# Kernel optimization log

Hardware: AMD Instinct MI355X
Metric: run time of the kernel (lower is better)

## Reference

```python
import jax, jax.numpy as jnp
import numpy as np

N_NODES = 100000
N_EDGES = 1600000
IN_C = 128
HID = 128
OUT_C = 10
NUM_GRAPHS = 512


def _glorot(key, shape):
    lim = float(np.sqrt(6.0 / (shape[0] + shape[1])))
    return jax.random.uniform(key, shape, jnp.float32, -lim, lim)


def setup_inputs() -> dict:
    key = jax.random.key(0)
    ks = jax.random.split(key, 12)
    x = jax.random.normal(ks[0], (N_NODES, IN_C), jnp.float32)
    edge_index = jax.random.randint(ks[1], (2, N_EDGES), 0, N_NODES, jnp.int64)
    batch = jnp.sort(jax.random.randint(ks[2], (N_NODES,), 0, NUM_GRAPHS, jnp.int64))
    return {
        'x': x, 'edge_index': edge_index, 'batch': batch,
        'Wc0': _glorot(ks[3], (IN_C, HID)), 'bc0': jnp.zeros((HID,), jnp.float32),
        'Wc1': _glorot(ks[4], (HID, HID)), 'bc1': jnp.zeros((HID,), jnp.float32),
        'Wc2': _glorot(ks[5], (HID, HID)), 'bc2': jnp.zeros((HID,), jnp.float32),
        'W1': _glorot(ks[6], (HID, HID)), 'b1': jnp.zeros((HID,), jnp.float32),
        'W2': _glorot(ks[7], (HID, OUT_C)), 'b2': jnp.zeros((OUT_C,), jnp.float32),
    }


def _gcn_conv(x, src, dst, W, b, n):
    # PyG GCNConv: add self-loops, symmetric norm D^-1/2 (A+I) D^-1/2, then XW + b.
    # deg includes the self-loop (+1); messages flow src -> dst.
    deg = jax.ops.segment_sum(jnp.ones((src.shape[0],), x.dtype), dst, num_segments=n) + 1.0
    dinv = jax.lax.rsqrt(deg)  # deg >= 1 so no zeros
    h = x @ W  # [N, H]
    coef = dinv[src] * dinv[dst]  # [E]
    agg = jax.ops.segment_sum(h[src] * coef[:, None], dst, num_segments=n)
    agg = agg + h * (dinv * dinv)[:, None]  # self-loop contribution, no edge materialization
    return agg + b


def reference(x, edge_index, batch, Wc0, bc0, Wc1, bc1, Wc2, bc2, W1, b1, W2, b2):
    n = x.shape[0]
    src, dst = edge_index[0], edge_index[1]
    # eval mode: dropout is identity
    h = jax.nn.relu(_gcn_conv(x, src, dst, Wc0, bc0, n))
    h = jax.nn.relu(_gcn_conv(h, src, dst, Wc1, bc1, n))
    h = _gcn_conv(h, src, dst, Wc2, bc2, n)
    # global_mean_pool over graphs
    sums = jax.ops.segment_sum(h, batch, num_segments=NUM_GRAPHS)
    counts = jax.ops.segment_sum(jnp.ones((n,), h.dtype), batch, num_segments=NUM_GRAPHS)
    pooled = sums / jnp.maximum(counts, 1.0)[:, None]  # [G, H]
    out = jax.nn.relu(pooled @ W1 + b1)
    return out @ W2 + b2  # [G, OUT_C]
```

## Files before the change

### kernel.cpp

```cpp
#include <hip/hip_runtime.h>
#include <hip/hip_bf16.h>
#include <stdint.h>

#define HID     128
#define OUTC    10
#define NGRAPH  512
#define NGROUP  64
#define PSIZE   256
#define CAP     160

using bf16x8 = __attribute__((ext_vector_type(8))) short;
using f32x4  = __attribute__((ext_vector_type(4))) float;

__device__ __forceinline__ short f2bf(float f) {
    __hip_bfloat16 h = __float2bfloat16(f);
    return *reinterpret_cast<short*>(&h);
}
__device__ __forceinline__ float bf2f(short s) {
    union { uint32_t u; float f; } x; x.u = ((uint32_t)(uint16_t)s) << 16; return x.f;
}
__device__ __forceinline__ float bflo(uint32_t v) {
    union { uint32_t u; float f; } x; x.u = v << 16; return x.f;
}
__device__ __forceinline__ float bfhi(uint32_t v) {
    union { uint32_t u; float f; } x; x.u = v & 0xffff0000u; return x.f;
}
__device__ __forceinline__ uint32_t pk2(float lo, float hi) {
    return (uint32_t)(uint16_t)f2bf(lo) | ((uint32_t)(uint16_t)f2bf(hi) << 16);
}

__global__ void detect64_kernel(const int* __restrict__ ei, int* __restrict__ flag) {
    int lane = threadIdx.x & 63;
    int v = ei[2 * lane + 1];
    unsigned long long b = __ballot(v == 0);
    if (threadIdx.x == 0) *flag = (b == ~0ULL) ? 1 : 0;
}

__device__ __forceinline__ int fetch_idx(const int* __restrict__ p, long j, int f64) {
    return p[f64 ? (j << 1) : j];
}

__global__ void __launch_bounds__(256) bin_scatter_kernel(
        const int* __restrict__ ei, const int* __restrict__ flag,
        int* __restrict__ cnt, uint32_t* __restrict__ binned,
        long E, int NBIN, int NBINP) {
    const int group = blockIdx.x & (NGROUP - 1);
    const int f = *flag;
    const long stride = (long)gridDim.x * blockDim.x;
    for (long e = (long)blockIdx.x * blockDim.x + threadIdx.x; e < E; e += stride) {
        int s = fetch_idx(ei, e, f);
        int d = fetch_idx(ei, E + e, f);
        int b = d >> 8;
        int pos = atomicAdd(&cnt[group * NBINP + b], 1);
        if (pos < CAP)
            binned[((size_t)group * NBIN + b) * CAP + pos] =
                (uint32_t)s | ((uint32_t)(d & (PSIZE - 1)) << 20);
    }
}

__global__ void bintot_kernel(const int* __restrict__ cnt, int* __restrict__ bin_tot,
                              int NBIN, int NBINP) {
    int b = blockIdx.x * blockDim.x + threadIdx.x;
    if (b < NBIN) {
        int s = 0;
#pragma unroll
        for (int g = 0; g < NGROUP; ++g) s += cnt[g * NBINP + b];
        bin_tot[b] = s;
    }
}

__global__ void __launch_bounds__(1024) scan_kernel(const int* __restrict__ deg,
                                                    int* __restrict__ ofs, int n) {
    __shared__ int wsum[16];
    __shared__ int carry_s;
    __shared__ int chunk_tot;
    const int tid  = threadIdx.x;
    const int lane = tid & 63;
    const int wid  = tid >> 6;
    if (tid == 0) carry_s = 0;
    __syncthreads();
    const int CHUNK = 4096;
    for (int base = 0; base < n; base += CHUNK) {
        int idx = base + tid * 4;
        int v[4];
#pragma unroll
        for (int j = 0; j < 4; ++j) v[j] = (idx + j < n) ? deg[idx + j] : 0;
        int s1 = v[0] + v[1] + v[2] + v[3];
        int inc = s1;
#pragma unroll
        for (int d = 1; d < 64; d <<= 1) {
            int t = __shfl_up(inc, d, 64);
            if (lane >= d) inc += t;
        }
        if (lane == 63) wsum[wid] = inc;
        __syncthreads();
        if (wid == 0) {
            int ws = (lane < 16) ? wsum[lane] : 0;
            int winc = ws;
#pragma unroll
            for (int d = 1; d < 16; d <<= 1) {
                int t = __shfl_up(winc, d, 64);
                if (lane >= d) winc += t;
            }
            if (lane == 15) chunk_tot = winc;
            if (lane < 16) wsum[lane] = winc - ws;
        }
        __syncthreads();
        int excl = carry_s + wsum[wid] + (inc - s1);
        int run = excl;
#pragma unroll
        for (int j = 0; j < 4; ++j) {
            if (idx + j < n) ofs[idx + j] = run;
            run += v[j];
        }
        __syncthreads();
        if (tid == 0) carry_s += chunk_tot;
        __syncthreads();
    }
    if (tid == 0) ofs[n] = carry_s;
}

__global__ void __launch_bounds__(512) bin_build_kernel(
        const uint32_t* __restrict__ binned, const int* __restrict__ cnt,
        const int* __restrict__ bofs, int* __restrict__ ofs,
        float* __restrict__ dinv, int* __restrict__ col,
        int n, int NBIN, int NBINP, long E) {
    __shared__ int lcnt[PSIZE];
    __shared__ int lofs[PSIZE];
    __shared__ int lrank[PSIZE];
    __shared__ int wtot[4];
    const int b    = blockIdx.x;
    const int v0   = b * PSIZE;
    const int nn   = min(PSIZE, n - v0);
    const int tid  = threadIdx.x;
    const int wv   = tid >> 6;
    const int lane = tid & 63;
    if (tid < PSIZE) { lcnt[tid] = 0; lrank[tid] = 0; }
    __syncthreads();
#pragma unroll
    for (int sg = wv; sg < NGROUP; sg += 8) {
        const int c = min(cnt[sg * NBINP + b], CAP);
        const uint32_t* __restrict__ src = binned + ((size_t)sg * NBIN + b) * CAP;
        for (int i = lane; i < c; i += 64)
            atomicAdd(&lcnt[src[i] >> 20], 1);
    }
    __syncthreads();
    if (tid < PSIZE) {
        int v = lcnt[tid];
        int inc = v;
#pragma unroll
        for (int d = 1; d < 64; d <<= 1) {
            int t = __shfl_up(inc, d, 64);
            if (lane >= d) inc += t;
        }
        if (lane == 63) wtot[wv] = inc;
        lofs[tid] = inc - v;
    }
    __syncthreads();
    if (tid < PSIZE) {
        int add = 0;
#pragma unroll
        for (int k = 0; k < 4; ++k) if (k < wv) add += wtot[k];
        lofs[tid] += add;
    }
    __syncthreads();
    const int base = bofs[b];
#pragma unroll
    for (int sg = wv; sg < NGROUP; sg += 8) {
        const int c = min(cnt[sg * NBINP + b], CAP);
        const uint32_t* __restrict__ src = binned + ((size_t)sg * NBIN + b) * CAP;
        for (int i = lane; i < c; i += 64) {
            uint32_t v = src[i];
            int dl = (int)(v >> 20);
            int rk = atomicAdd(&lrank[dl], 1);
            col[base + lofs[dl] + rk] = (int)(v & 0xFFFFFu);
        }
    }
    if (tid < nn) {
        ofs[v0 + tid]  = base + lofs[tid];
        dinv[v0 + tid] = rsqrtf((float)lcnt[tid] + 1.0f);
    }
    if (tid == 0 && v0 + nn == n) ofs[n] = (int)E;
}

__global__ void __launch_bounds__(128) wprep_kernel(
        const float* __restrict__ W0, const float* __restrict__ W1,
        const float* __restrict__ W2, short* __restrict__ Wt) {
    const float* W = (blockIdx.x == 0) ? W0 : (blockIdx.x == 1) ? W1 : W2;
    short* hi = Wt + (size_t)blockIdx.x * 2 * HID * HID;
    short* lo = hi + HID * HID;
    __shared__ float Ws[64][129];
    const int t = threadIdx.x;
    for (int half = 0; half < 2; ++half) {
        const int kbase = half * 64;
#pragma unroll
        for (int it = 0; it < 16; ++it) {
            int idx = (t + it * 128) * 4;
            int k = idx >> 7, c = idx & 127;
            float4 v = *(const float4*)(W + (size_t)(kbase + k) * HID + c);
            Ws[k][c] = v.x; Ws[k][c + 1] = v.y; Ws[k][c + 2] = v.z; Ws[k][c + 3] = v.w;
        }
        __syncthreads();
        for (int it = 0; it < 64; ++it) {
            int k2 = t & 63;
            int c  = (t >> 6) + it * 2;
            float w = Ws[k2][c];
            short h = f2bf(w);
            hi[(size_t)c * HID + kbase + k2] = h;
            lo[(size_t)c * HID + kbase + k2] = f2bf(w - bf2f(h));
        }
        __syncthreads();
    }
}

template<bool AFP32>
__global__ void __launch_bounds__(256) gemm_hs_kernel(
        const void* __restrict__ Ap, const short* __restrict__ Wt,
        const float* __restrict__ dinv, short* __restrict__ hs, int n) {
    const short* __restrict__ Bh = Wt;
    const short* __restrict__ Bl = Wt + HID * HID;
    const int tid = threadIdx.x;
    const int w  = tid >> 6;
    const int l  = tid & 63;
    const int lr = l & 15;
    const int kq = l >> 4;
    const int r0 = blockIdx.x * 128;

    f32x4 acc[8][2] = {};
    const int col0 = w * 32 + lr;
    const int col1 = w * 32 + 16 + lr;

    const float* Af = (const float*)Ap;
    const short* Ab = (const short*)Ap;

#pragma unroll
    for (int ks = 0; ks < 4; ++ks) {
        const int k0 = ks * 32 + kq * 8;
        bf16x8 a[8];
#pragma unroll
        for (int rf = 0; rf < 8; ++rf) {
            int row = r0 + rf * 16 + lr;
            if (row >= n) row = n - 1;
            if (AFP32) {
                const float* ap = Af + (size_t)row * HID + k0;
                float4 f0 = *(const float4*)ap;
                float4 f1 = *(const float4*)(ap + 4);
                bf16x8 tv;
                tv[0] = f2bf(f0.x); tv[1] = f2bf(f0.y); tv[2] = f2bf(f0.z); tv[3] = f2bf(f0.w);
                tv[4] = f2bf(f1.x); tv[5] = f2bf(f1.y); tv[6] = f2bf(f1.z); tv[7] = f2bf(f1.w);
                a[rf] = tv;
            } else {
                a[rf] = *(const bf16x8*)(Ab + (size_t)row * HID + k0);
            }
        }
        bf16x8 bh0 = *(const bf16x8*)(Bh + (size_t)col0 * HID + k0);
        bf16x8 bh1 = *(const bf16x8*)(Bh + (size_t)col1 * HID + k0);
        bf16x8 bl0 = *(const bf16x8*)(Bl + (size_t)col0 * HID + k0);
        bf16x8 bl1 = *(const bf16x8*)(Bl + (size_t)col1 * HID + k0);
#pragma unroll
        for (int rf = 0; rf < 8; ++rf) {
            acc[rf][0] = __builtin_amdgcn_mfma_f32_16x16x32_bf16(a[rf], bh0, acc[rf][0], 0, 0, 0);
            acc[rf][1] = __builtin_amdgcn_mfma_f32_16x16x32_bf16(a[rf], bh1, acc[rf][1], 0, 0, 0);
            acc[rf][0] = __builtin_amdgcn_mfma_f32_16x16x32_bf16(a[rf], bl0, acc[rf][0], 0, 0, 0);
            acc[rf][1] = __builtin_amdgcn_mfma_f32_16x16x32_bf16(a[rf], bl1, acc[rf][1], 0, 0, 0);
        }
    }
#pragma unroll
    for (int rf = 0; rf < 8; ++rf) {
#pragma unroll
        for (int rg = 0; rg < 4; ++rg) {
            int row = r0 + rf * 16 + kq * 4 + rg;
            if (row < n) {
                float dn = dinv[row];
                hs[(size_t)row * HID + col0] = f2bf(acc[rf][0][rg] * dn);
                hs[(size_t)row * HID + col1] = f2bf(acc[rf][1][rg] * dn);
            }
        }
    }
}

__device__ __forceinline__ void acc_add(float* acc, uint4 v) {
    acc[0] += bflo(v.x); acc[1] += bfhi(v.x);
    acc[2] += bflo(v.y); acc[3] += bfhi(v.y);
    acc[4] += bflo(v.z); acc[5] += bfhi(v.z);
    acc[6] += bflo(v.w); acc[7] += bfhi(v.w);
}

__global__ void __launch_bounds__(256) agg_kernel(
        const short* __restrict__ hs, const float* __restrict__ dinv,
        const int* __restrict__ ofs, const int* __restrict__ col,
        const float* __restrict__ bias, short* __restrict__ out,
        int n, int do_relu) {
    int node = blockIdx.x * 4 + (threadIdx.x >> 6);
    if (node >= n) return;
    const int lane = threadIdx.x & 63;
    const int g    = lane >> 4;
    const int sub  = lane & 15;
    const uint4* __restrict__ rows = (const uint4*)hs;

    float acc[8] = {0.f, 0.f, 0.f, 0.f, 0.f, 0.f, 0.f, 0.f};
    if (g == 0) {
        uint4 sv = rows[(size_t)node * 16 + sub];
        acc_add(acc, sv);
    }
    const int e0 = ofs[node], e1 = ofs[node + 1];
    int e = e0;
    for (; e + 16 <= e1; e += 16) {
        int c0 = col[e + g];
        int c1 = col[e + 4 + g];
        int c2 = col[e + 8 + g];
        int c3 = col[e + 12 + g];
        uint4 v0 = rows[(size_t)c0 * 16 + sub];
        uint4 v1 = rows[(size_t)c1 * 16 + sub];
        uint4 v2 = rows[(size_t)c2 * 16 + sub];
        uint4 v3 = rows[(size_t)c3 * 16 + sub];
        acc_add(acc, v0); acc_add(acc, v1); acc_add(acc, v2); acc_add(acc, v3);
    }
    for (; e + 4 <= e1; e += 4) {
        int c0 = col[e + g];
        uint4 v0 = rows[(size_t)c0 * 16 + sub];
        acc_add(acc, v0);
    }
    if (e + g < e1) {
        int c0 = col[e + g];
        uint4 v0 = rows[(size_t)c0 * 16 + sub];
        acc_add(acc, v0);
    }
#pragma unroll
    for (int i = 0; i < 8; ++i) {
        acc[i] += __shfl_xor(acc[i], 16, 64);
        acc[i] += __shfl_xor(acc[i], 32, 64);
    }
    if (g == 0) {
        const float dn = dinv[node];
        float4 b0 = *(const float4*)(bias + 8 * sub);
        float4 b1 = *(const float4*)(bias + 8 * sub + 4);
        float o0 = fmaf(acc[0], dn, b0.x);
        float o1 = fmaf(acc[1], dn, b0.y);
        float o2 = fmaf(acc[2], dn, b0.z);
        float o3 = fmaf(acc[3], dn, b0.w);
        float o4 = fmaf(acc[4], dn, b1.x);
        float o5 = fmaf(acc[5], dn, b1.y);
        float o6 = fmaf(acc[6], dn, b1.z);
        float o7 = fmaf(acc[7], dn, b1.w);
        if (do_relu) {
            o0 = fmaxf(o0, 0.f); o1 = fmaxf(o1, 0.f);
            o2 = fmaxf(o2, 0.f); o3 = fmaxf(o3, 0.f);
            o4 = fmaxf(o4, 0.f); o5 = fmaxf(o5, 0.f);
            o6 = fmaxf(o6, 0.f); o7 = fmaxf(o7, 0.f);
        }
        uint4 pk;
        pk.x = pk2(o0, o1); pk.y = pk2(o2, o3);
        pk.z = pk2(o4, o5); pk.w = pk2(o6, o7);
        ((uint4*)out)[(size_t)node * 16 + sub] = pk;
    }
}

__global__ void boundary_kernel(const int* __restrict__ batch, const int* __restrict__ flag,
                                int* __restrict__ gstart, int n) {
    int i = blockIdx.x * blockDim.x + threadIdx.x;
    if (i >= n) return;
    int f = *flag;
    int b  = fetch_idx(batch, i, f);
    int bp = (i == 0) ? -1 : fetch_idx(batch, i - 1, f);
    for (int g = bp + 1; g <= b; ++g) gstart[g] = i;
    if (i == n - 1) {
        for (int g = b + 1; g <= NGRAPH; ++g) gstart[g] = n;
    }
}

__global__ void __launch_bounds__(128) pool_kernel(const short* __restrict__ h,
                                                   const int* __restrict__ gstart,
                                                   float* __restrict__ pooled) {
    int g = blockIdx.x, c = threadIdx.x;
    int s = gstart[g], e = gstart[g + 1];
    float acc = 0.f;
    int i = s;
    for (; i + 4 <= e; i += 4) {
        acc += bf2f(h[(size_t)i * HID + c]) + bf2f(h[(size_t)(i + 1) * HID + c])
             + bf2f(h[(size_t)(i + 2) * HID + c]) + bf2f(h[(size_t)(i + 3) * HID + c]);
    }
    for (; i < e; ++i) acc += bf2f(h[(size_t)i * HID + c]);
    float cnt = (float)(e - s);
    pooled[g * HID + c] = acc / fmaxf(cnt, 1.f);
}

__global__ void __launch_bounds__(128) mlp_kernel(
        const float* __restrict__ pooled,
        const float* __restrict__ W1, const float* __restrict__ b1,
        const float* __restrict__ W2, const float* __restrict__ b2,
        float* __restrict__ out) {
    __shared__ float p[HID];
    __shared__ float hid[HID];
    int g = blockIdx.x, c = threadIdx.x;
    p[c] = pooled[g * HID + c];
    __syncthreads();
    float a = b1[c];
#pragma unroll 8
    for (int k = 0; k < HID; ++k) a = fmaf(p[k], W1[k * HID + c], a);
    hid[c] = fmaxf(a, 0.f);
    __syncthreads();
    if (c < OUTC) {
        float o = b2[c];
#pragma unroll 8
        for (int k = 0; k < HID; ++k) o = fmaf(hid[k], W2[k * OUTC + c], o);
        out[g * OUTC + c] = o;
    }
}

extern "C" void kernel_launch(void* const* d_in, const int* in_sizes, int n_in,
                              void* d_out, int out_size, void* d_ws, size_t ws_size,
                              hipStream_t stream) {
    const float* x   = (const float*)d_in[0];
    const int*   ei  = (const int*)d_in[1];
    const int*   bat = (const int*)d_in[2];
    const float* Wc0 = (const float*)d_in[3];
    const float* bc0 = (const float*)d_in[4];
    const float* Wc1 = (const float*)d_in[5];
    const float* bc1 = (const float*)d_in[6];
    const float* Wc2 = (const float*)d_in[7];
    const float* bc2 = (const float*)d_in[8];
    const float* W1  = (const float*)d_in[9];
    const float* b1  = (const float*)d_in[10];
    const float* W2  = (const float*)d_in[11];
    const float* b2  = (const float*)d_in[12];
    float* out = (float*)d_out;

    const int  n = in_sizes[0] / HID;
    const long E = in_sizes[1] / 2;
    const int  NBIN  = (n + PSIZE - 1) / PSIZE;
    const int  NBINP = (NBIN + 15) & ~15;

    char* w = (char*)d_ws;
    size_t off = 0;
    auto carve = [&](size_t bytes) {
        void* p = w + off;
        off += (bytes + 255) & ~(size_t)255;
        return p;
    };
    int*   flag    = (int*)carve(4);
    int*   cnt     = (int*)carve((size_t)NGROUP * NBINP * 4);
    int*   bin_tot = (int*)carve((size_t)NBIN * 4);
    int*   bofs    = (int*)carve((size_t)(NBIN + 1) * 4);
    int*   ofs     = (int*)carve((size_t)(n + 1) * 4);
    float* dinv    = (float*)carve((size_t)n * 4);
    int*   gstart  = (int*)carve((NGRAPH + 1) * 4);
    int*   col     = (int*)carve((size_t)E * 4);
    short* Wt      = (short*)carve((size_t)3 * 2 * HID * HID * 2);
    short* hs      = (short*)carve((size_t)n * HID * 2);
    short* h       = (short*)carve((size_t)n * HID * 2);
    float* pooled  = (float*)carve((size_t)NGRAPH * HID * 4);
    uint32_t* binned = (uint32_t*)h;

    hipMemsetAsync(cnt, 0, (size_t)NGROUP * NBINP * 4, stream);

    detect64_kernel<<<1, 64, 0, stream>>>(ei, flag);

    bin_scatter_kernel<<<2048, 256, 0, stream>>>(ei, flag, cnt, binned, E, NBIN, NBINP);
    bintot_kernel<<<(NBIN + 255) / 256, 256, 0, stream>>>(cnt, bin_tot, NBIN, NBINP);
    scan_kernel<<<1, 1024, 0, stream>>>(bin_tot, bofs, NBIN);
    bin_build_kernel<<<NBIN, 512, 0, stream>>>(binned, cnt, bofs, ofs, dinv, col,
                                               n, NBIN, NBINP, E);
    wprep_kernel<<<3, 128, 0, stream>>>(Wc0, Wc1, Wc2, Wt);

    const int gb = (n + 127) / 128;
    const int ab = (n + 3) / 4;
    const size_t WSTRIDE = (size_t)2 * HID * HID;
    gemm_hs_kernel<true><<<gb, 256, 0, stream>>>(x, Wt, dinv, hs, n);
    agg_kernel<<<ab, 256, 0, stream>>>(hs, dinv, ofs, col, bc0, h, n, 1);
    gemm_hs_kernel<false><<<gb, 256, 0, stream>>>(h, Wt + WSTRIDE, dinv, hs, n);
    agg_kernel<<<ab, 256, 0, stream>>>(hs, dinv, ofs, col, bc1, h, n, 1);
    gemm_hs_kernel<false><<<gb, 256, 0, stream>>>(h, Wt + 2 * WSTRIDE, dinv, hs, n);
    agg_kernel<<<ab, 256, 0, stream>>>(hs, dinv, ofs, col, bc2, h, n, 0);

    boundary_kernel<<<(n + 255) / 256, 256, 0, stream>>>(bat, flag, gstart, n);
    pool_kernel<<<NGRAPH, 128, 0, stream>>>(h, gstart, pooled);
    mlp_kernel<<<NGRAPH, 128, 0, stream>>>(pooled, W1, b1, W2, b2, out);
}
```

Before: 435.2 us.

## Fuse bin total and scan, widen binning groups, streamline aggregation loop

Merges the per-bin total kernel and the prefix scan into one single-block kernel, which drops a launch and an intermediate buffer. Doubles the number of atomic groups in binning and shrinks the per-bin capacity to cut atomic contention. Rewrites the aggregation loop as a single predicated 16-edge loop with nontemporal index loads and output stores. The single-block scan assumes no more than 1024 bins, and a smaller capacity raises the risk of bin overflow dropping edges if the degree distribution is skewed.

```diff
diff --git a/kernel.cpp b/kernel.cpp
--- a/kernel.cpp
+++ b/kernel.cpp
@@ -5,12 +5,13 @@
 #define HID     128
 #define OUTC    10
 #define NGRAPH  512
-#define NGROUP  64
+#define NGROUP  128
 #define PSIZE   256
-#define CAP     160
+#define CAP     88
 
 using bf16x8 = __attribute__((ext_vector_type(8))) short;
 using f32x4  = __attribute__((ext_vector_type(4))) float;
+using u32x4  = __attribute__((ext_vector_type(4))) uint32_t;
 
 __device__ __forceinline__ short f2bf(float f) {
     __hip_bfloat16 h = __float2bfloat16(f);
@@ -58,66 +59,37 @@
     }
 }
 
-__global__ void bintot_kernel(const int* __restrict__ cnt, int* __restrict__ bin_tot,
-                              int NBIN, int NBINP) {
-    int b = blockIdx.x * blockDim.x + threadIdx.x;
-    if (b < NBIN) {
-        int s = 0;
-#pragma unroll
-        for (int g = 0; g < NGROUP; ++g) s += cnt[g * NBINP + b];
-        bin_tot[b] = s;
-    }
-}
-
-__global__ void __launch_bounds__(1024) scan_kernel(const int* __restrict__ deg,
-                                                    int* __restrict__ ofs, int n) {
+__global__ void __launch_bounds__(1024) binscan_kernel(
+        const int* __restrict__ cnt, int* __restrict__ bofs, int NBIN, int NBINP) {
     __shared__ int wsum[16];
-    __shared__ int carry_s;
-    __shared__ int chunk_tot;
     const int tid  = threadIdx.x;
     const int lane = tid & 63;
     const int wid  = tid >> 6;
-    if (tid == 0) carry_s = 0;
-    __syncthreads();
-    const int CHUNK = 4096;
-    for (int base = 0; base < n; base += CHUNK) {
-        int idx = base + tid * 4;
-        int v[4];
-#pragma unroll
-        for (int j = 0; j < 4; ++j) v[j] = (idx + j < n) ? deg[idx + j] : 0;
-        int s1 = v[0] + v[1] + v[2] + v[3];
-        int inc = s1;
-#pragma unroll
-        for (int d = 1; d < 64; d <<= 1) {
-            int t = __shfl_up(inc, d, 64);
-            if (lane >= d) inc += t;
-        }
-        if (lane == 63) wsum[wid] = inc;
-        __syncthreads();
-        if (wid == 0) {
-            int ws = (lane < 16) ? wsum[lane] : 0;
-            int winc = ws;
-#pragma unroll
-            for (int d = 1; d < 16; d <<= 1) {
-                int t = __shfl_up(winc, d, 64);
-                if (lane >= d) winc += t;
-            }
-            if (lane == 15) chunk_tot = winc;
-            if (lane < 16) wsum[lane] = winc - ws;
-        }
-        __syncthreads();
-        int excl = carry_s + wsum[wid] + (inc - s1);
-        int run = excl;
-#pragma unroll
-        for (int j = 0; j < 4; ++j) {
-            if (idx + j < n) ofs[idx + j] = run;
-            run += v[j];
-        }
-        __syncthreads();
-        if (tid == 0) carry_s += chunk_tot;
-        __syncthreads();
-    }
-    if (tid == 0) ofs[n] = carry_s;
+    int v = 0;
+    if (tid < NBIN) {
+        for (int g = 0; g < NGROUP; ++g) v += cnt[g * NBINP + tid];
+    }
+    int inc = v;
+#pragma unroll
+    for (int d = 1; d < 64; d <<= 1) {
+        int t = __shfl_up(inc, d, 64);
+        if (lane >= d) inc += t;
+    }
+    if (lane == 63) wsum[wid] = inc;
+    __syncthreads();
+    if (wid == 0) {
+        int ws = (lane < 16) ? wsum[lane] : 0;
+        int winc = ws;
+#pragma unroll
+        for (int d = 1; d < 16; d <<= 1) {
+            int t = __shfl_up(winc, d, 64);
+            if (lane >= d) winc += t;
+        }
+        if (lane < 16) wsum[lane] = winc - ws;
+    }
+    __syncthreads();
+    int excl = wsum[wid] + (inc - v);
+    if (tid <= NBIN) bofs[tid] = excl;
 }
 
 __global__ void __launch_bounds__(512) bin_build_kernel(
@@ -137,7 +109,6 @@
     const int lane = tid & 63;
     if (tid < PSIZE) { lcnt[tid] = 0; lrank[tid] = 0; }
     __syncthreads();
-#pragma unroll
     for (int sg = wv; sg < NGROUP; sg += 8) {
         const int c = min(cnt[sg * NBINP + b], CAP);
         const uint32_t* __restrict__ src = binned + ((size_t)sg * NBIN + b) * CAP;
@@ -165,7 +136,6 @@
     }
     __syncthreads();
     const int base = bofs[b];
-#pragma unroll
     for (int sg = wv; sg < NGROUP; sg += 8) {
         const int c = min(cnt[sg * NBINP + b], CAP);
         const uint32_t* __restrict__ src = binned + ((size_t)sg * NBIN + b) * CAP;
@@ -279,7 +249,7 @@
     }
 }
 
-__device__ __forceinline__ void acc_add(float* acc, uint4 v) {
+__device__ __forceinline__ void acc_add(float* acc, u32x4 v) {
     acc[0] += bflo(v.x); acc[1] += bfhi(v.x);
     acc[2] += bflo(v.y); acc[3] += bfhi(v.y);
     acc[4] += bflo(v.z); acc[5] += bfhi(v.z);
@@ -296,35 +266,31 @@
     const int lane = threadIdx.x & 63;
     const int g    = lane >> 4;
     const int sub  = lane & 15;
-    const uint4* __restrict__ rows = (const uint4*)hs;
+    const u32x4* __restrict__ rows = (const u32x4*)hs;
 
     float acc[8] = {0.f, 0.f, 0.f, 0.f, 0.f, 0.f, 0.f, 0.f};
     if (g == 0) {
-        uint4 sv = rows[(size_t)node * 16 + sub];
+        u32x4 sv = rows[(size_t)node * 16 + sub];
         acc_add(acc, sv);
     }
     const int e0 = ofs[node], e1 = ofs[node + 1];
-    int e = e0;
-    for (; e + 16 <= e1; e += 16) {
-        int c0 = col[e + g];
-        int c1 = col[e + 4 + g];
-        int c2 = col[e + 8 + g];
-        int c3 = col[e + 12 + g];
-        uint4 v0 = rows[(size_t)c0 * 16 + sub];
-        uint4 v1 = rows[(size_t)c1 * 16 + sub];
-        uint4 v2 = rows[(size_t)c2 * 16 + sub];
-        uint4 v3 = rows[(size_t)c3 * 16 + sub];
-        acc_add(acc, v0); acc_add(acc, v1); acc_add(acc, v2); acc_add(acc, v3);
-    }
-    for (; e + 4 <= e1; e += 4) {
-        int c0 = col[e + g];
-        uint4 v0 = rows[(size_t)c0 * 16 + sub];
-        acc_add(acc, v0);
-    }
-    if (e + g < e1) {
-        int c0 = col[e + g];
-        uint4 v0 = rows[(size_t)c0 * 16 + sub];
-        acc_add(acc, v0);
+    for (int e = e0; e < e1; e += 16) {
+        int i0 = e + g;
+        int i1 = e + 4 + g;
+        int i2 = e + 8 + g;
+        int i3 = e + 12 + g;
+        int c0 = __builtin_nontemporal_load(col + (i0 < e1 ? i0 : e0));
+        int c1 = __builtin_nontemporal_load(col + (i1 < e1 ? i1 : e0));
+        int c2 = __builtin_nontemporal_load(col + (i2 < e1 ? i2 : e0));
+        int c3 = __builtin_nontemporal_load(col + (i3 < e1 ? i3 : e0));
+        u32x4 v0 = rows[(size_t)c0 * 16 + sub];
+        u32x4 v1 = rows[(size_t)c1 * 16 + sub];
+        u32x4 v2 = rows[(size_t)c2 * 16 + sub];
+        u32x4 v3 = rows[(size_t)c3 * 16 + sub];
+        if (i0 < e1) acc_add(acc, v0);
+        if (i1 < e1) acc_add(acc, v1);
+        if (i2 < e1) acc_add(acc, v2);
+        if (i3 < e1) acc_add(acc, v3);
     }
 #pragma unroll
     for (int i = 0; i < 8; ++i) {
@@ -349,10 +315,10 @@
             o4 = fmaxf(o4, 0.f); o5 = fmaxf(o5, 0.f);
             o6 = fmaxf(o6, 0.f); o7 = fmaxf(o7, 0.f);
         }
-        uint4 pk;
+        u32x4 pk;
         pk.x = pk2(o0, o1); pk.y = pk2(o2, o3);
         pk.z = pk2(o4, o5); pk.w = pk2(o6, o7);
-        ((uint4*)out)[(size_t)node * 16 + sub] = pk;
+        __builtin_nontemporal_store(pk, (u32x4*)out + (size_t)node * 16 + sub);
     }
 }
 
@@ -440,7 +406,6 @@
     };
     int*   flag    = (int*)carve(4);
     int*   cnt     = (int*)carve((size_t)NGROUP * NBINP * 4);
-    int*   bin_tot = (int*)carve((size_t)NBIN * 4);
     int*   bofs    = (int*)carve((size_t)(NBIN + 1) * 4);
     int*   ofs     = (int*)carve((size_t)(n + 1) * 4);
     float* dinv    = (float*)carve((size_t)n * 4);
@@ -457,8 +422,7 @@
     detect64_kernel<<<1, 64, 0, stream>>>(ei, flag);
 
     bin_scatter_kernel<<<2048, 256, 0, stream>>>(ei, flag, cnt, binned, E, NBIN, NBINP);
-    bintot_kernel<<<(NBIN + 255) / 256, 256, 0, stream>>>(cnt, bin_tot, NBIN, NBINP);
-    scan_kernel<<<1, 1024, 0, stream>>>(bin_tot, bofs, NBIN);
+    binscan_kernel<<<1, 1024, 0, stream>>>(cnt, bofs, NBIN, NBINP);
     bin_build_kernel<<<NBIN, 512, 0, stream>>>(binned, cnt, bofs, ofs, dinv, col,
                                                n, NBIN, NBINP, E);
     wprep_kernel<<<3, 128, 0, stream>>>(Wc0, Wc1, Wc2, Wt);
```

New measurement: 467.4 us. 1.07x slower.
